# Optimization experiments

Hardware: AMD Instinct MI355X
Metric: run time of the kernel (lower is better)

## Reference

```python
import jax, jax.numpy as jnp
import numpy as np

EPS = 1e-12  # torch F.normalize eps

def _l2norm(v, axis):
    n = jnp.linalg.norm(v, axis=axis, keepdims=True)
    return v / jnp.maximum(n, EPS)

def setup_inputs() -> dict:
    key = jax.random.key(0)
    k1, k2, k3 = jax.random.split(key, 3)
    N, D, H, W, K = 32, 512, 40, 40, 64
    x = jax.random.normal(k1, (N, D, H, W), dtype=jnp.float32)
    conv_weight = jax.random.normal(k2, (K, D), dtype=jnp.float32) * 0.05
    centroids = jax.random.uniform(k3, (K, D), dtype=jnp.float32)
    return {"x": x, "conv_weight": conv_weight, "centroids": centroids}

def reference(x, conv_weight, centroids):
    N, D, H, W = x.shape
    K = centroids.shape[0]
    # descriptor-wise L2 normalization over channel dim
    x = _l2norm(x, axis=1)
    x_flat = x.reshape(N, D, H * W)                       # [N, D, S]
    # 1x1 conv == per-pixel linear: [K,D] @ [N,D,S] -> [N,K,S]
    logits = jnp.einsum('kd,nds->nks', conv_weight, x_flat)
    soft_assign = jax.nn.softmax(logits, axis=1)          # softmax over clusters
    # vlad[n,k,d] = sum_s a[n,k,s] * (x[n,d,s] - c[k,d])
    #            = (a @ x^T) - (sum_s a) * c   -- two GEMM-like ops, no K-loop
    agg = jnp.einsum('nks,nds->nkd', soft_assign, x_flat)  # [N, K, D]
    a_sum = soft_assign.sum(axis=2)                        # [N, K]
    vlad = agg - a_sum[:, :, None] * centroids[None, :, :]
    # intra-normalization over D, flatten, global L2 normalization
    vlad = _l2norm(vlad, axis=2)
    vlad = vlad.reshape(N, K * D)
    vlad = _l2norm(vlad, axis=1)
    return vlad
```

## Files before the change

kernel.cpp:

```cpp
#include <hip/hip_runtime.h>
#include <math.h>

#define N_ 32
#define D_ 512
#define S_ 1600
#define K_ 64

typedef __attribute__((ext_vector_type(8))) short short8;
typedef __attribute__((ext_vector_type(4))) float f32x4;

static __device__ __forceinline__ short f2bf(float f) {
    unsigned u = __float_as_uint(f);
    u += 0x7fffu + ((u >> 16) & 1u);
    return (short)(u >> 16);
}

__global__ __launch_bounds__(256) void kW(const float* __restrict__ w,
                                          short* __restrict__ w16)
{
    int i4 = (blockIdx.x * 256 + threadIdx.x) * 4;
    float4 v = *(const float4*)&w[i4];
    short4 h = {f2bf(v.x), f2bf(v.y), f2bf(v.z), f2bf(v.w)};
    *(short4*)&w16[i4] = h;
}

__global__ __launch_bounds__(64) void kA(const float* __restrict__ x,
                                         const short* __restrict__ w16,
                                         short* __restrict__ aprime,
                                         float* __restrict__ asum)
{
    const int l   = threadIdx.x;
    const int lk  = l & 15;
    const int q   = l >> 4;
    const int n   = blockIdx.x / 100;
    const int s0w = (blockIdx.x % 100) * 16;

    const float* xcol = x + (size_t)n * D_ * S_ + s0w + lk;

    f32x4 accl[4];
#pragma unroll
    for (int kt = 0; kt < 4; ++kt) accl[kt] = (f32x4){0.f, 0.f, 0.f, 0.f};
    float ssq = 0.f;

#pragma unroll 2
    for (int kst = 0; kst < 16; ++kst) {
        float xv[8];
#pragma unroll
        for (int j = 0; j < 8; ++j)
            xv[j] = xcol[(size_t)(kst * 32 + q * 8 + j) * S_];
        short8 bf;
#pragma unroll
        for (int j = 0; j < 8; ++j) {
            ssq += xv[j] * xv[j];
            bf[j] = f2bf(xv[j]);
        }
#pragma unroll
        for (int kt = 0; kt < 4; ++kt) {
            short8 af = *(const short8*)&w16[(size_t)(kt * 16 + lk) * D_ + kst * 32 + q * 8];
            accl[kt] = __builtin_amdgcn_mfma_f32_16x16x32_bf16(af, bf, accl[kt], 0, 0, 0);
        }
    }

    ssq += __shfl_xor(ssq, 16);
    ssq += __shfl_xor(ssq, 32);
    const float inv = 1.0f / fmaxf(sqrtf(ssq), 1e-12f);

    float e[4][4];
    float sm = 0.f;
#pragma unroll
    for (int kt = 0; kt < 4; ++kt)
#pragma unroll
        for (int r = 0; r < 4; ++r) {
            e[kt][r] = __expf(accl[kt][r] * inv);
            sm += e[kt][r];
        }
    sm += __shfl_xor(sm, 16);
    sm += __shfl_xor(sm, 32);
    const float rs = 1.0f / sm;

    short* apb = aprime + (size_t)n * K_ * S_ + s0w + lk;
#pragma unroll
    for (int kt = 0; kt < 4; ++kt)
#pragma unroll
        for (int r = 0; r < 4; ++r) {
            const float p = e[kt][r] * rs;
            apb[(size_t)(kt * 16 + 4 * q + r) * S_] = f2bf(p * inv);
            float v = p;
            v += __shfl_xor(v, 1);
            v += __shfl_xor(v, 2);
            v += __shfl_xor(v, 4);
            v += __shfl_xor(v, 8);
            if (lk == 0) atomicAdd(&asum[n * K_ + kt * 16 + 4 * q + r], v);
        }
}

__global__ __launch_bounds__(256) void kB(const float* __restrict__ x,
                                          const short* __restrict__ aprime,
                                          float* __restrict__ agg)
{
    const int bid = blockIdx.x;
    const int n  = bid / 20;
    const int dt = (bid % 20) / 5;
    const int sp = bid % 5;
    const int wv = threadIdx.x >> 6;
    const int l  = threadIdx.x & 63;
    const int lk = l & 15;
    const int q  = l >> 4;
    const int dbase = dt * 128 + wv * 32;

    const short* ap = aprime + (size_t)n * K_ * S_;
    const float* xb = x + (size_t)n * D_ * S_;

    f32x4 acc[4][2];
#pragma unroll
    for (int kt = 0; kt < 4; ++kt)
#pragma unroll
        for (int ds = 0; ds < 2; ++ds) acc[kt][ds] = (f32x4){0.f, 0.f, 0.f, 0.f};

    for (int kst = 0; kst < 10; ++kst) {
        const int s = sp * 320 + kst * 32 + q * 8;
        short8 af[4];
#pragma unroll
        for (int kt = 0; kt < 4; ++kt)
            af[kt] = *(const short8*)&ap[(size_t)(kt * 16 + lk) * S_ + s];
        short8 bf[2];
#pragma unroll
        for (int ds = 0; ds < 2; ++ds) {
            const float* xp = &xb[(size_t)(dbase + ds * 16 + lk) * S_ + s];
            float4 v0 = *(const float4*)xp;
            float4 v1 = *(const float4*)(xp + 4);
            short8 b;
            b[0] = f2bf(v0.x); b[1] = f2bf(v0.y); b[2] = f2bf(v0.z); b[3] = f2bf(v0.w);
            b[4] = f2bf(v1.x); b[5] = f2bf(v1.y); b[6] = f2bf(v1.z); b[7] = f2bf(v1.w);
            bf[ds] = b;
        }
#pragma unroll
        for (int kt = 0; kt < 4; ++kt)
#pragma unroll
            for (int ds = 0; ds < 2; ++ds)
                acc[kt][ds] = __builtin_amdgcn_mfma_f32_16x16x32_bf16(af[kt], bf[ds], acc[kt][ds], 0, 0, 0);
    }

    float* ab = agg + (size_t)n * K_ * D_;
#pragma unroll
    for (int kt = 0; kt < 4; ++kt)
#pragma unroll
        for (int ds = 0; ds < 2; ++ds)
#pragma unroll
            for (int r = 0; r < 4; ++r)
                atomicAdd(&ab[(size_t)(kt * 16 + 4 * q + r) * D_ + dbase + ds * 16 + lk],
                          acc[kt][ds][r]);
}

__global__ __launch_bounds__(256) void kC(const float* __restrict__ agg,
                                          const float* __restrict__ asum,
                                          const float* __restrict__ cent,
                                          float* __restrict__ out)
{
    __shared__ float red[4];
    const int tid = threadIdx.x;
    const int nk = blockIdx.x;
    const int k = nk & 63;
    const float as = asum[nk];
    const float* cb = cent + (size_t)k * D_;
    const float* ag = agg + (size_t)nk * D_;

    float v0 = ag[tid]       - as * cb[tid];
    float v1 = ag[tid + 256] - as * cb[tid + 256];
    float ssq = v0 * v0 + v1 * v1;

    ssq += __shfl_xor(ssq, 32);
    ssq += __shfl_xor(ssq, 16);
    ssq += __shfl_xor(ssq, 8);
    ssq += __shfl_xor(ssq, 4);
    ssq += __shfl_xor(ssq, 2);
    ssq += __shfl_xor(ssq, 1);
    if ((tid & 63) == 0) red[tid >> 6] = ssq;
    __syncthreads();
    const float total = red[0] + red[1] + red[2] + red[3];
    const float scale = 1.0f / (fmaxf(sqrtf(total), 1e-12f) * 8.0f);

    out[(size_t)nk * D_ + tid]       = v0 * scale;
    out[(size_t)nk * D_ + tid + 256] = v1 * scale;
}

extern "C" void kernel_launch(void* const* d_in, const int* in_sizes, int n_in,
                              void* d_out, int out_size, void* d_ws, size_t ws_size,
                              hipStream_t stream)
{
    const float* x    = (const float*)d_in[0];
    const float* w    = (const float*)d_in[1];
    const float* cent = (const float*)d_in[2];
    float* out = (float*)d_out;

    float* agg    = (float*)d_ws;
    float* asum   = agg + (size_t)N_ * K_ * D_;
    short* aprime = (short*)(asum + N_ * K_);
    short* w16    = aprime + (size_t)N_ * K_ * S_;

    hipMemsetAsync(agg, 0, ((size_t)N_ * K_ * D_ + N_ * K_) * sizeof(float), stream);

    kW<<<32, 256, 0, stream>>>(w, w16);
    kA<<<N_ * (S_ / 16), 64, 0, stream>>>(x, w16, aprime, asum);
    kB<<<N_ * 4 * 5, 256, 0, stream>>>(x, aprime, agg);
    kC<<<N_ * K_, 256, 0, stream>>>(agg, asum, cent, out);
}
```

Measured before the change: 222.2 us.

## Split kA channel reduction across four waves with LDS partial-sum combine

kA now uses 256 threads per block, with each wave covering a quarter of the 512 channels for the same 16 pixels. Partial logits and the squared-norm partials go to shared memory and are summed after a barrier. Each wave then does the softmax and writes one 16-cluster slice of the assignments and sums. This cuts the serial dependent loads and MFMA chain per wave and adds memory-level parallelism, at the cost of LDS traffic, a barrier, and redundant softmax/exp work in every wave.

Result: slower. 236.3 us (+6.4%).

```diff
diff --git a/kernel.cpp b/kernel.cpp
--- a/kernel.cpp
+++ b/kernel.cpp
@@ -24,12 +24,16 @@
     *(short4*)&w16[i4] = h;
 }
 
-__global__ __launch_bounds__(64) void kA(const float* __restrict__ x,
-                                         const short* __restrict__ w16,
-                                         short* __restrict__ aprime,
-                                         float* __restrict__ asum)
-{
-    const int l   = threadIdx.x;
+__global__ __launch_bounds__(256) void kA(const float* __restrict__ x,
+                                          const short* __restrict__ w16,
+                                          short* __restrict__ aprime,
+                                          float* __restrict__ asum)
+{
+    __shared__ float pacc[4][64][17];
+
+    const int tid = threadIdx.x;
+    const int wv  = tid >> 6;
+    const int l   = tid & 63;
     const int lk  = l & 15;
     const int q   = l >> 4;
     const int n   = blockIdx.x / 100;
@@ -42,12 +46,13 @@
     for (int kt = 0; kt < 4; ++kt) accl[kt] = (f32x4){0.f, 0.f, 0.f, 0.f};
     float ssq = 0.f;
 
-#pragma unroll 2
-    for (int kst = 0; kst < 16; ++kst) {
+#pragma unroll
+    for (int kst = 0; kst < 4; ++kst) {
+        const int d0 = wv * 128 + kst * 32 + q * 8;
         float xv[8];
 #pragma unroll
         for (int j = 0; j < 8; ++j)
-            xv[j] = xcol[(size_t)(kst * 32 + q * 8 + j) * S_];
+            xv[j] = xcol[(size_t)(d0 + j) * S_];
         short8 bf;
 #pragma unroll
         for (int j = 0; j < 8; ++j) {
@@ -56,42 +61,57 @@
         }
 #pragma unroll
         for (int kt = 0; kt < 4; ++kt) {
-            short8 af = *(const short8*)&w16[(size_t)(kt * 16 + lk) * D_ + kst * 32 + q * 8];
+            short8 af = *(const short8*)&w16[(size_t)(kt * 16 + lk) * D_ + d0];
             accl[kt] = __builtin_amdgcn_mfma_f32_16x16x32_bf16(af, bf, accl[kt], 0, 0, 0);
         }
     }
 
-    ssq += __shfl_xor(ssq, 16);
-    ssq += __shfl_xor(ssq, 32);
-    const float inv = 1.0f / fmaxf(sqrtf(ssq), 1e-12f);
-
-    float e[4][4];
+#pragma unroll
+    for (int kt = 0; kt < 4; ++kt)
+#pragma unroll
+        for (int r = 0; r < 4; ++r)
+            pacc[wv][l][kt * 4 + r] = accl[kt][r];
+    pacc[wv][l][16] = ssq;
+    __syncthreads();
+
+    float tot[16];
+#pragma unroll
+    for (int i = 0; i < 16; ++i) tot[i] = pacc[0][l][i];
+    float tssq = pacc[0][l][16];
+#pragma unroll
+    for (int w2 = 1; w2 < 4; ++w2) {
+#pragma unroll
+        for (int i = 0; i < 16; ++i) tot[i] += pacc[w2][l][i];
+        tssq += pacc[w2][l][16];
+    }
+
+    tssq += __shfl_xor(tssq, 16);
+    tssq += __shfl_xor(tssq, 32);
+    const float inv = 1.0f / fmaxf(sqrtf(tssq), 1e-12f);
+
+    float e[16];
     float sm = 0.f;
 #pragma unroll
-    for (int kt = 0; kt < 4; ++kt)
-#pragma unroll
-        for (int r = 0; r < 4; ++r) {
-            e[kt][r] = __expf(accl[kt][r] * inv);
-            sm += e[kt][r];
-        }
+    for (int i = 0; i < 16; ++i) {
+        e[i] = __expf(tot[i] * inv);
+        sm += e[i];
+    }
     sm += __shfl_xor(sm, 16);
     sm += __shfl_xor(sm, 32);
     const float rs = 1.0f / sm;
 
     short* apb = aprime + (size_t)n * K_ * S_ + s0w + lk;
 #pragma unroll
-    for (int kt = 0; kt < 4; ++kt)
-#pragma unroll
-        for (int r = 0; r < 4; ++r) {
-            const float p = e[kt][r] * rs;
-            apb[(size_t)(kt * 16 + 4 * q + r) * S_] = f2bf(p * inv);
-            float v = p;
-            v += __shfl_xor(v, 1);
-            v += __shfl_xor(v, 2);
-            v += __shfl_xor(v, 4);
-            v += __shfl_xor(v, 8);
-            if (lk == 0) atomicAdd(&asum[n * K_ + kt * 16 + 4 * q + r], v);
-        }
+    for (int r = 0; r < 4; ++r) {
+        const float p = e[wv * 4 + r] * rs;
+        apb[(size_t)(16 * wv + 4 * q + r) * S_] = f2bf(p * inv);
+        float v = p;
+        v += __shfl_xor(v, 1);
+        v += __shfl_xor(v, 2);
+        v += __shfl_xor(v, 4);
+        v += __shfl_xor(v, 8);
+        if (lk == 0) atomicAdd(&asum[n * K_ + 16 * wv + 4 * q + r], v);
+    }
 }
 
 __global__ __launch_bounds__(256) void kB(const float* __restrict__ x,
@@ -201,7 +221,7 @@
     hipMemsetAsync(agg, 0, ((size_t)N_ * K_ * D_ + N_ * K_) * sizeof(float), stream);
 
     kW<<<32, 256, 0, stream>>>(w, w16);
-    kA<<<N_ * (S_ / 16), 64, 0, stream>>>(x, w16, aprime, asum);
+    kA<<<N_ * (S_ / 16), 256, 0, stream>>>(x, w16, aprime, asum);
     kB<<<N_ * 4 * 5, 256, 0, stream>>>(x, aprime, agg);
     kC<<<N_ * K_, 256, 0, stream>>>(agg, asum, cent, out);
 }
```
